# Kernel tuning notes

Hardware: AMD Instinct MI355X
Metric: run time of the kernel (lower is better)

## Reference

```python
import jax, jax.numpy as jnp
import numpy as np

NEG_INF = -9e15  # matches torch's -9000000000000000.0 mask value
LEAKY_SLOPE = 0.2  # alpha init arg


def setup_inputs() -> dict:
    key = jax.random.key(0)
    k1, k2, k3, k4, k5, k6 = jax.random.split(key, 6)
    B, N, D = 512, 200, 256
    hidden = jax.random.normal(k1, (B, N, D), dtype=jnp.float32)
    adj = jax.random.randint(k2, (B, N, N), 0, 5, dtype=jnp.int32)
    a0 = jax.random.normal(k3, (D,), dtype=jnp.float32)
    a1 = jax.random.normal(k4, (D,), dtype=jnp.float32)
    a2 = jax.random.normal(k5, (D,), dtype=jnp.float32)
    a3 = jax.random.normal(k6, (D,), dtype=jnp.float32)
    return {"hidden": hidden, "adj": adj, "a0": a0, "a1": a1, "a2": a2, "a3": a3}


def reference(hidden, adj, a0, a1, a2, a3):
    # e_k[b,i,j] = leakyrelu( sum_d h[b,i,d] * h[b,j,d] * a_k[d] )
    # Algebraically identical to the torch (h_i * h_j) @ a_k without
    # materializing the [B, N, N, D] pairwise product tensor.
    def edge_score(a):
        s = jnp.einsum('bid,bjd->bij', hidden * a, hidden)
        return jax.nn.leaky_relu(s, LEAKY_SLOPE)

    e0, e1, e2, e3 = edge_score(a0), edge_score(a1), edge_score(a2), edge_score(a3)
    alpha = jnp.where(adj == 1, e0, NEG_INF)
    alpha = jnp.where(adj == 2, e1, alpha)
    alpha = jnp.where(adj == 3, e2, alpha)
    alpha = jnp.where(adj == 4, e3, alpha)
    alpha = jax.nn.softmax(alpha, axis=-1)  # [B, N, N]
    return jnp.matmul(alpha, hidden)  # [B, N, D]
```

## Files before the change

kernel.cpp:

```cpp
#include <hip/hip_runtime.h>

#define NB 512
#define NN 200
#define ND 256
#define TI 40
#define DC 32
#define NTILE 5
#define NEG_INF -9.0e15f
#define SLOPE 0.2f

#define HJ_STRIDE 205
#define WI_STRIDE 44

__global__ __launch_bounds__(512, 4)
void gat_fused_w_kernel(const float* __restrict__ h,
                        const int*   __restrict__ adj,
                        const float* __restrict__ a0,
                        const float* __restrict__ a1,
                        const float* __restrict__ a2,
                        const float* __restrict__ a3,
                        float* __restrict__ out)
{
    __shared__ float sHjT[DC][HJ_STRIDE];
    __shared__ float sW[4][DC][WI_STRIDE];
    __shared__ float sS[TI][NN];

    const int tid = threadIdx.x;
    const int b   = blockIdx.x / NTILE;
    const int it  = blockIdx.x % NTILE;
    const int i0  = it * TI;

    const int ig = tid / 50;
    const int jg = tid % 50;
    const bool active = (ig < 10);

    const float* hb = h + (size_t)b * NN * ND;

    int kk[4][4];
    if (active) {
        #pragma unroll
        for (int ii = 0; ii < 4; ++ii) {
            const int i = i0 + ig * 4 + ii;
            const int* arow = adj + ((size_t)b * NN + i) * NN;
            #pragma unroll
            for (int jj = 0; jj < 4; ++jj)
                kk[ii][jj] = arow[jg + 50 * jj] - 1;
        }
    }

    float acc[4][4][4];
    #pragma unroll
    for (int ii = 0; ii < 4; ++ii)
        #pragma unroll
        for (int jj = 0; jj < 4; ++jj)
            #pragma unroll
            for (int k = 0; k < 4; ++k)
                acc[ii][jj][k] = 0.0f;

    for (int dt = 0; dt < ND; dt += DC) {
        {
            const int row = tid >> 3;
            const int c4  = (tid & 7) * 4;
            for (int j = row; j < NN; j += 64) {
                const float4 v = *(const float4*)(hb + j * ND + dt + c4);
                sHjT[c4 + 0][j] = v.x;
                sHjT[c4 + 1][j] = v.y;
                sHjT[c4 + 2][j] = v.z;
                sHjT[c4 + 3][j] = v.w;
            }
            for (int r = row; r < TI; r += 64) {
                const float4 hv  = *(const float4*)(hb + (i0 + r) * ND + dt + c4);
                const float4 va0 = *(const float4*)(a0 + dt + c4);
                const float4 va1 = *(const float4*)(a1 + dt + c4);
                const float4 va2 = *(const float4*)(a2 + dt + c4);
                const float4 va3 = *(const float4*)(a3 + dt + c4);
                sW[0][c4 + 0][r] = hv.x * va0.x;
                sW[0][c4 + 1][r] = hv.y * va0.y;
                sW[0][c4 + 2][r] = hv.z * va0.z;
                sW[0][c4 + 3][r] = hv.w * va0.w;
                sW[1][c4 + 0][r] = hv.x * va1.x;
                sW[1][c4 + 1][r] = hv.y * va1.y;
                sW[1][c4 + 2][r] = hv.z * va1.z;
                sW[1][c4 + 3][r] = hv.w * va1.w;
                sW[2][c4 + 0][r] = hv.x * va2.x;
                sW[2][c4 + 1][r] = hv.y * va2.y;
                sW[2][c4 + 2][r] = hv.z * va2.z;
                sW[2][c4 + 3][r] = hv.w * va2.w;
                sW[3][c4 + 0][r] = hv.x * va3.x;
                sW[3][c4 + 1][r] = hv.y * va3.y;
                sW[3][c4 + 2][r] = hv.z * va3.z;
                sW[3][c4 + 3][r] = hv.w * va3.w;
            }
        }
        __syncthreads();

        if (active) {
            #pragma unroll 4
            for (int dd = 0; dd < DC; ++dd) {
                float hjv[4];
                #pragma unroll
                for (int jj = 0; jj < 4; ++jj) hjv[jj] = sHjT[dd][jg + 50 * jj];
                #pragma unroll
                for (int k = 0; k < 4; ++k) {
                    float wv_[4];
                    #pragma unroll
                    for (int ii = 0; ii < 4; ++ii) wv_[ii] = sW[k][dd][ig * 4 + ii];
                    #pragma unroll
                    for (int ii = 0; ii < 4; ++ii)
                        #pragma unroll
                        for (int jj = 0; jj < 4; ++jj)
                            acc[ii][jj][k] += wv_[ii] * hjv[jj];
                }
            }
        }
        __syncthreads();
    }

    if (active) {
        #pragma unroll
        for (int ii = 0; ii < 4; ++ii) {
            #pragma unroll
            for (int jj = 0; jj < 4; ++jj) {
                const int k = kk[ii][jj];
                float s = (k < 2) ? ((k == 0) ? acc[ii][jj][0] : acc[ii][jj][1])
                                  : ((k == 2) ? acc[ii][jj][2] : acc[ii][jj][3]);
                s = (s >= 0.0f) ? s : SLOPE * s;
                s = (k >= 0) ? s : NEG_INF;
                sS[ig * 4 + ii][jg + 50 * jj] = s;
            }
        }
    }
    __syncthreads();

    const int wv   = tid >> 6;
    const int lane = tid & 63;
    #pragma unroll
    for (int r = 0; r < 5; ++r) {
        const int row = wv * 5 + r;
        const float v0 = sS[row][lane];
        const float v1 = sS[row][lane + 64];
        const float v2 = sS[row][lane + 128];
        const float v3 = (lane < 8) ? sS[row][lane + 192] : NEG_INF;
        float m = fmaxf(fmaxf(v0, v1), fmaxf(v2, v3));
        #pragma unroll
        for (int off = 32; off > 0; off >>= 1)
            m = fmaxf(m, __shfl_xor(m, off, 64));
        const float p0 = __expf(v0 - m);
        const float p1 = __expf(v1 - m);
        const float p2 = __expf(v2 - m);
        const float p3 = (lane < 8) ? __expf(v3 - m) : 0.0f;
        float l = p0 + p1 + p2 + p3;
        #pragma unroll
        for (int off = 32; off > 0; off >>= 1)
            l += __shfl_xor(l, off, 64);
        const float inv = 1.0f / l;
        sS[row][lane]       = p0 * inv;
        sS[row][lane + 64]  = p1 * inv;
        sS[row][lane + 128] = p2 * inv;
        if (lane < 8) sS[row][lane + 192] = p3 * inv;
    }
    __syncthreads();

    float o[5][4];
    #pragma unroll
    for (int r = 0; r < 5; ++r)
        #pragma unroll
        for (int c = 0; c < 4; ++c)
            o[r][c] = 0.0f;

    const int dcol = lane * 4;
    #pragma unroll 4
    for (int j = 0; j < NN; ++j) {
        const float4 hv = *(const float4*)(hb + j * ND + dcol);
        #pragma unroll
        for (int r = 0; r < 5; ++r) {
            const float al = sS[wv * 5 + r][j];
            o[r][0] += al * hv.x;
            o[r][1] += al * hv.y;
            o[r][2] += al * hv.z;
            o[r][3] += al * hv.w;
        }
    }

    #pragma unroll
    for (int r = 0; r < 5; ++r) {
        const int i = i0 + wv * 5 + r;
        float4 v;
        v.x = o[r][0]; v.y = o[r][1]; v.z = o[r][2]; v.w = o[r][3];
        *(float4*)(out + ((size_t)b * NN + i) * ND + dcol) = v;
    }
}

extern "C" void kernel_launch(void* const* d_in, const int* in_sizes, int n_in,
                              void* d_out, int out_size, void* d_ws, size_t ws_size,
                              hipStream_t stream) {
    const float* h   = (const float*)d_in[0];
    const int*   adj = (const int*)d_in[1];
    const float* a0  = (const float*)d_in[2];
    const float* a1  = (const float*)d_in[3];
    const float* a2  = (const float*)d_in[4];
    const float* a3  = (const float*)d_in[5];
    float* out = (float*)d_out;

    dim3 grid(NB * NTILE);
    dim3 block(512);
    gat_fused_w_kernel<<<grid, block, 0, stream>>>(h, adj, a0, a1, a2, a3, out);
}
```

Measured before the change: 730.1 us.

## Vectorize shared-memory accesses with contiguous per-thread columns and alias LDS buffers

Each thread now owns four contiguous j columns instead of columns strided by 50. This lets adjacency loads, sHjT reads, sW reads and score writes use 128-bit int4/float4 accesses, and the stride becomes 204 so rows stay 16-byte aligned. The score buffer is aliased onto the staging buffers to shrink LDS use, and the alpha@h loop reads four alpha values per float4 from shared memory. The intent is fewer LDS instructions and higher occupancy, at the risk of more bank conflicts with contiguous float4 patterns.

Result: faster. 651.0 us (-10.8%).

```diff
diff --git a/kernel.cpp b/kernel.cpp
--- a/kernel.cpp
+++ b/kernel.cpp
@@ -9,21 +9,25 @@
 #define NEG_INF -9.0e15f
 #define SLOPE 0.2f
 
-#define HJ_STRIDE 205
+#define HJ_STRIDE 204
 #define WI_STRIDE 44
+#define P1_HJ (DC * HJ_STRIDE)
+#define P1_W  (4 * DC * WI_STRIDE)
+#define POOLF (P1_HJ + P1_W)
 
 __global__ __launch_bounds__(512, 4)
-void gat_fused_w_kernel(const float* __restrict__ h,
-                        const int*   __restrict__ adj,
-                        const float* __restrict__ a0,
-                        const float* __restrict__ a1,
-                        const float* __restrict__ a2,
-                        const float* __restrict__ a3,
-                        float* __restrict__ out)
+void gat_fused_w2_kernel(const float* __restrict__ h,
+                         const int*   __restrict__ adj,
+                         const float* __restrict__ a0,
+                         const float* __restrict__ a1,
+                         const float* __restrict__ a2,
+                         const float* __restrict__ a3,
+                         float* __restrict__ out)
 {
-    __shared__ float sHjT[DC][HJ_STRIDE];
-    __shared__ float sW[4][DC][WI_STRIDE];
-    __shared__ float sS[TI][NN];
+    __shared__ __align__(16) float pool[POOLF];
+    float (*sHjT)[HJ_STRIDE]   = (float (*)[HJ_STRIDE])pool;
+    float (*sW)[DC][WI_STRIDE] = (float (*)[DC][WI_STRIDE])(pool + P1_HJ);
+    float (*sS)[NN]            = (float (*)[NN])pool;
 
     const int tid = threadIdx.x;
     const int b   = blockIdx.x / NTILE;
@@ -41,10 +45,11 @@
         #pragma unroll
         for (int ii = 0; ii < 4; ++ii) {
             const int i = i0 + ig * 4 + ii;
-            const int* arow = adj + ((size_t)b * NN + i) * NN;
-            #pragma unroll
-            for (int jj = 0; jj < 4; ++jj)
-                kk[ii][jj] = arow[jg + 50 * jj] - 1;
+            const int4 a4 = *(const int4*)(adj + ((size_t)b * NN + i) * NN + 4 * jg);
+            kk[ii][0] = a4.x - 1;
+            kk[ii][1] = a4.y - 1;
+            kk[ii][2] = a4.z - 1;
+            kk[ii][3] = a4.w - 1;
         }
     }
 
@@ -97,14 +102,12 @@
         if (active) {
             #pragma unroll 4
             for (int dd = 0; dd < DC; ++dd) {
-                float hjv[4];
-                #pragma unroll
-                for (int jj = 0; jj < 4; ++jj) hjv[jj] = sHjT[dd][jg + 50 * jj];
+                const float4 hj4 = *(const float4*)&sHjT[dd][4 * jg];
+                const float hjv[4] = {hj4.x, hj4.y, hj4.z, hj4.w};
                 #pragma unroll
                 for (int k = 0; k < 4; ++k) {
-                    float wv_[4];
-                    #pragma unroll
-                    for (int ii = 0; ii < 4; ++ii) wv_[ii] = sW[k][dd][ig * 4 + ii];
+                    const float4 w4 = *(const float4*)&sW[k][dd][4 * ig];
+                    const float wv_[4] = {w4.x, w4.y, w4.z, w4.w};
                     #pragma unroll
                     for (int ii = 0; ii < 4; ++ii)
                         #pragma unroll
@@ -119,15 +122,18 @@
     if (active) {
         #pragma unroll
         for (int ii = 0; ii < 4; ++ii) {
+            float tmp[4];
             #pragma unroll
             for (int jj = 0; jj < 4; ++jj) {
                 const int k = kk[ii][jj];
                 float s = (k < 2) ? ((k == 0) ? acc[ii][jj][0] : acc[ii][jj][1])
                                   : ((k == 2) ? acc[ii][jj][2] : acc[ii][jj][3]);
                 s = (s >= 0.0f) ? s : SLOPE * s;
-                s = (k >= 0) ? s : NEG_INF;
-                sS[ig * 4 + ii][jg + 50 * jj] = s;
-            }
+                tmp[jj] = (k >= 0) ? s : NEG_INF;
+            }
+            float4 sv;
+            sv.x = tmp[0]; sv.y = tmp[1]; sv.z = tmp[2]; sv.w = tmp[3];
+            *(float4*)&sS[ig * 4 + ii][4 * jg] = sv;
         }
     }
     __syncthreads();
@@ -169,16 +175,24 @@
             o[r][c] = 0.0f;
 
     const int dcol = lane * 4;
-    #pragma unroll 4
-    for (int j = 0; j < NN; ++j) {
-        const float4 hv = *(const float4*)(hb + j * ND + dcol);
+    #pragma unroll 2
+    for (int j4 = 0; j4 < NN / 4; ++j4) {
+        float alr[5][4];
         #pragma unroll
         for (int r = 0; r < 5; ++r) {
-            const float al = sS[wv * 5 + r][j];
-            o[r][0] += al * hv.x;
-            o[r][1] += al * hv.y;
-            o[r][2] += al * hv.z;
-            o[r][3] += al * hv.w;
+            const float4 a4 = *(const float4*)&sS[wv * 5 + r][4 * j4];
+            alr[r][0] = a4.x; alr[r][1] = a4.y; alr[r][2] = a4.z; alr[r][3] = a4.w;
+        }
+        #pragma unroll
+        for (int q = 0; q < 4; ++q) {
+            const float4 hv = *(const float4*)(hb + (size_t)(4 * j4 + q) * ND + dcol);
+            #pragma unroll
+            for (int r = 0; r < 5; ++r) {
+                o[r][0] += alr[r][q] * hv.x;
+                o[r][1] += alr[r][q] * hv.y;
+                o[r][2] += alr[r][q] * hv.z;
+                o[r][3] += alr[r][q] * hv.w;
+            }
         }
     }
 
@@ -204,5 +218,5 @@
 
     dim3 grid(NB * NTILE);
     dim3 block(512);
-    gat_fused_w_kernel<<<grid, block, 0, stream>>>(h, adj, a0, a1, a2, a3, out);
+    gat_fused_w2_kernel<<<grid, block, 0, stream>>>(h, adj, a0, a1, a2, a3, out);
 }
```
